# Kernel tuning notes

Hardware: AMD Instinct MI355X
Metric: run time of the kernel (lower is better)

The kernel has to match this reference:

```python
import jax, jax.numpy as jnp
import numpy as np

VOCAB = 128
N_LAYERS = 4
HEAD_DIM = 128
N_HEADS = 16
PAD = 127
HIDDEN = N_HEADS * HEAD_DIM
B, S = 1, 2048
SCALE = 1.0 / float(np.sqrt(HEAD_DIM))


def _intervals(boundary):
    # torch: interval = cumsum(boundary)+1; shifted = roll(1); shifted[:,0]=interval[:,0]
    idx = jnp.cumsum(boundary.astype(jnp.int32), axis=-1) + 1
    sh = jnp.roll(idx, 1, axis=-1)
    return sh.at[:, 0].set(idx[:, 0])


def _build_mask(tokens, segment_mask, specials_mask):
    # Combined causal & padding & word & segment mask, cache_size=0, distances=0.
    word_int = _intervals(specials_mask)            # [B,S]
    seg_bound = ~segment_mask                       # [B,S]
    seg_int = _intervals(seg_bound)                 # [B,S]
    q = jnp.arange(S)[:, None]
    kv = jnp.arange(S)[None, :]
    causal = q >= kv                                # [S,S]
    dist_neg = (q - kv) < 0                         # mask_*_distance = 0 term
    nonpad = tokens != PAD                          # [B,S]
    padm = nonpad[:, :, None] & nonpad[:, None, :]  # [B,S,S]
    wordm = specials_mask[:, None, :] | dist_neg[None] | (word_int[:, :, None] == word_int[:, None, :])
    segm = seg_bound[:, None, :] | dist_neg[None] | (seg_int[:, :, None] == seg_int[:, None, :])
    return causal[None] & padm & wordm & segm       # [B,S,S]


def _attention(h, mask):
    # q=k=v=h (no projections in DummyModel); flex_attention default scale 1/sqrt(D)
    x = h.reshape(B, S, N_HEADS, HEAD_DIM)
    scores = jnp.einsum('bqhd,bkhd->bhqk', x, x) * SCALE
    neg = jnp.finfo(scores.dtype).min
    scores = jnp.where(mask[:, None], scores, neg)
    probs = jax.nn.softmax(scores, axis=-1)
    # fully-masked rows (e.g. padding queries) -> zero output, matching flex_attention
    row_valid = jnp.any(mask, axis=-1)              # [B,S]
    probs = jnp.where(row_valid[:, None, :, None], probs, 0.0)
    out = jnp.einsum('bhqk,bkhd->bqhd', probs, x)
    return out.reshape(B, S, HIDDEN)


def setup_inputs() -> dict:
    key = jax.random.key(0)
    k1, k2, k3, k4, k5, k6 = jax.random.split(key, 6)
    tokens = jax.random.randint(k1, (B, S), 0, PAD)          # 0..126, no pad tokens
    segment_mask = jax.random.bernoulli(k2, 0.98, (B, S))
    specials_mask = jax.random.bernoulli(k3, 0.2, (B, S))    # True = word boundary/special
    emb_w = jax.random.normal(k4, (VOCAB, HIDDEN), jnp.float32) * 0.02
    lm_w = jax.random.normal(k5, (VOCAB, HIDDEN), jnp.float32) * 0.02
    lm_b = jnp.zeros((VOCAB,), jnp.float32)
    seg_w = jax.random.normal(k6, (2, HIDDEN), jnp.float32) * 0.02
    seg_b = jnp.zeros((2,), jnp.float32)
    return {"tokens": tokens, "segment_mask": segment_mask, "specials_mask": specials_mask,
            "emb_w": emb_w, "lm_w": lm_w, "lm_b": lm_b, "seg_w": seg_w, "seg_b": seg_b}


def reference(tokens, segment_mask, specials_mask, emb_w, lm_w, lm_b, seg_w, seg_b):
    mask = _build_mask(tokens, segment_mask, specials_mask)
    hidden = emb_w[tokens]                                   # [B,S,HIDDEN]
    for _ in range(N_LAYERS):
        hidden = _attention(hidden, mask)
    logits = hidden @ lm_w.T + lm_b                          # [B,S,VOCAB]
    logits_segment = hidden @ seg_w.T + seg_b                # [B,S,2]
    return logits, logits_segment
```

## Files before the change

### kernel.cpp

```cpp
#include <hip/hip_runtime.h>

#define S 2048
#define HID 2048
#define NH 16
#define DH 128
#define VOC 128
#define LCAP 128
#define K2EXP 0.12752551286084112f
#define RTHR 62.0f
#define NEGS -3.0e38f

typedef __bf16 bf16_t;
typedef __attribute__((ext_vector_type(8))) __bf16 bf16x8;
typedef __attribute__((ext_vector_type(4))) __bf16 bf16x4;
typedef __attribute__((ext_vector_type(4))) float f32x4;
typedef __attribute__((ext_vector_type(16))) float f32x16;

typedef __attribute__((address_space(1))) unsigned int guint;
typedef __attribute__((address_space(3))) unsigned int luint;

#define MFMA16 __builtin_amdgcn_mfma_f32_16x16x32_bf16
#define MFMA32 __builtin_amdgcn_mfma_f32_32x32x16_bf16

__device__ __forceinline__ void gl_lds16(const void* g, void* l) {
  __builtin_amdgcn_global_load_lds((guint*)(unsigned long long)g,
                                   (luint*)(unsigned)(unsigned long long)l,
                                   16, 0, 0);
}

__device__ __forceinline__ unsigned cvtpk(float lo, float hi) {
  unsigned r;
  asm("v_cvt_pk_bf16_f32 %0, %1, %2" : "=v"(r) : "v"(lo), "v"(hi));
  return r;
}
__device__ __forceinline__ void plswap(unsigned& a, unsigned& b) {
  asm volatile("v_permlane32_swap_b32 %0, %1" : "+v"(a), "+v"(b));
}
__device__ __forceinline__ bf16x8 mk8(unsigned d0, unsigned d1, unsigned d2, unsigned d3) {
  union { unsigned u[4]; bf16x8 v; } x;
  x.u[0] = d0; x.u[1] = d1; x.u[2] = d2; x.u[3] = d3;
  return x.v;
}

__global__ __launch_bounds__(256) void maskprep2(const int* __restrict__ tokens,
                                                 const unsigned char* __restrict__ seg,
                                                 const unsigned char* __restrict__ spc,
                                                 int4* __restrict__ mi,
                                                 int* __restrict__ lq,
                                                 unsigned long long* __restrict__ lmask,
                                                 int2* __restrict__ smeta) {
  __shared__ int ssp[257], ssg[257], smw[257], sms[257], sfl[257];
  __shared__ int fpre[2048];
  __shared__ int ns32[32];
  __shared__ unsigned long long lmk[32];
  __shared__ int cdet[2];
  int t = threadIdx.x;
  if (t < 2) cdet[t] = 0;
  if (t < 32) lmk[t] = 0ull;
  __syncthreads();
  {
    int nz = ((t & 3) != 0 && seg[t]) ? 1 : 0;
    int fc = ((t & 3) == 3 && seg[t] == 0x3f) ? 1 : 0;
    if (nz) atomicAdd(&cdet[0], 1);
    if (fc) atomicAdd(&cdet[1], 1);
  }
  __syncthreads();
  int lay = (cdet[1] > 8) ? 2 : ((cdet[0] > 4) ? 1 : 0);
  auto getb = [&](const unsigned char* p, int i) -> int {
    if (lay == 1) return p[i] != 0;
    if (lay == 2) return ((const float*)p)[i] != 0.f;
    return ((const int*)p)[i] != 0;
  };
  int base = t * 8;
  int spv[8], sgv[8], npv[8], fv[8];
  int a = 0, b = 0, mw = 0, ms = 0, fs = 0;
  for (int j = 0; j < 8; j++) {
    int i = base + j;
    spv[j] = getb(spc, i);
    sgv[j] = 1 - getb(seg, i);
    npv[j] = (tokens[i] != 127) ? 1 : 0;
    fv[j] = spv[j] & sgv[j] & npv[j];
    a += spv[j]; b += sgv[j]; fs += fv[j];
    if (i >= 1 && spv[j]) mw = (i + 1 > mw) ? i + 1 : mw;
    if (i >= 1 && sgv[j]) ms = (i + 1 > ms) ? i + 1 : ms;
  }
  ssp[t + 1] = a; ssg[t + 1] = b; smw[t + 1] = mw; sms[t + 1] = ms; sfl[t + 1] = fs;
  if (t == 0) { ssp[0] = 0; ssg[0] = 0; smw[0] = 0; sms[0] = 0; sfl[0] = 0; }
  __syncthreads();
  for (int off = 1; off < 256; off <<= 1) {
    int v0 = 0, v1 = 0, v2 = 0, v3 = 0, v4 = 0;
    if (t + 1 > off) { v0 = ssp[t+1-off]; v1 = ssg[t+1-off]; v2 = smw[t+1-off]; v3 = sms[t+1-off]; v4 = sfl[t+1-off]; }
    __syncthreads();
    ssp[t + 1] += v0; ssg[t + 1] += v1;
    if (v2 > smw[t + 1]) smw[t + 1] = v2;
    if (v3 > sms[t + 1]) sms[t + 1] = v3;
    sfl[t + 1] += v4;
    __syncthreads();
  }
  if ((t & 7) == 0) {
    int ws = smw[t], ss = sms[t];
    ns32[t >> 3] = ws < ss ? ws : ss;
  }
  int esp = ssp[t], esg = ssg[t], ef = sfl[t];
  for (int j = 0; j < 8; j++) {
    int i = base + j;
    int wint = (i == 0) ? (1 + spv[j]) : (1 + esp);
    int sint = (i == 0) ? (1 + sgv[j]) : (1 + esg);
    mi[i] = make_int4(npv[j] | (spv[j] << 1) | (sgv[j] << 2), wint, sint, 0);
    fpre[i] = ef;
    int lqv = (fv[j] && ef < LCAP) ? ef : -1;
    lq[i] = lqv;
    if (lqv >= 0) atomicOr(&lmk[i >> 6], 1ull << (i & 63));
    esp += spv[j]; esg += sgv[j]; ef += fv[j];
  }
  __syncthreads();
  if (t < 32) {
    lmask[t] = lmk[t];
    int nsTile = ns32[t] >> 6;
    int lc = fpre[nsTile * 64];
    if (lc > LCAP) lc = LCAP;
    smeta[t] = make_int2(nsTile, lc);
  }
}

__global__ __launch_bounds__(256) void bitgen(const int4* __restrict__ mi,
                                              unsigned* __restrict__ cmask) {
  __shared__ int4 km[32];
  int w = blockIdx.x;
  int t = threadIdx.x;
  int q = blockIdx.y * 256 + t;
  if (t < 32) km[t] = mi[w * 32 + t];
  __syncthreads();
  int4 mq = mi[q];
  unsigned word = 0;
  #pragma unroll
  for (int j = 0; j < 32; j++) {
    int kv = w * 32 + j;
    int4 mk = km[j];
    bool v = ((mq.x & mk.x) & 1) &&
             ((mk.x & 2) || (mq.y == mk.y)) &&
             ((mk.x & 4) || (mq.z == mk.z)) &&
             (kv <= q);
    word |= (v ? 1u : 0u) << j;
  }
  cmask[(size_t)w * S + q] = word;
}

__device__ __forceinline__ void store_h_hT(bf16x8 ob[4], bf16_t* tile, int q0, int h,
                                           int ql, int d0, int tid,
                                           bf16_t* __restrict__ hb, bf16_t* __restrict__ hbT) {
  #pragma unroll
  for (int i = 0; i < 4; i++)
    *(bf16x8*)(hb + (size_t)(q0 + ql) * HID + h * DH + d0 + i * 8) = ob[i];
  #pragma unroll
  for (int i = 0; i < 4; i++)
    #pragma unroll
    for (int j = 0; j < 8; j++) tile[ql * 136 + d0 + i * 8 + j] = ob[i][j];
  __syncthreads();
  int dT = tid >> 1, qh = (tid & 1) * 32;
  bf16x8 tb[4];
  #pragma unroll
  for (int i = 0; i < 4; i++)
    #pragma unroll
    for (int j = 0; j < 8; j++) tb[i][j] = tile[(qh + i * 8 + j) * 136 + dT];
  #pragma unroll
  for (int i = 0; i < 4; i++)
    *(bf16x8*)(hbT + (size_t)(h * DH + dT) * S + q0 + qh + i * 8) = tb[i];
}

__global__ __launch_bounds__(256) void embedT(const int* __restrict__ tokens,
                                              const float* __restrict__ emb,
                                              const int* __restrict__ lq,
                                              const unsigned long long* __restrict__ lmask,
                                              bf16_t* __restrict__ hb, bf16_t* __restrict__ hbT,
                                              bf16_t* __restrict__ hbL, bf16_t* __restrict__ hbLT) {
  __shared__ bf16_t tile[64 * 136];
  int tid = threadIdx.x;
  int q0 = blockIdx.x * 64, h = blockIdx.y;
  int ql = tid >> 2, d0 = (tid & 3) * 32;
  int tok = tokens[q0 + ql];
  const float4* src = (const float4*)(emb + (size_t)tok * HID + h * DH + d0);
  bf16x8 ob[4];
  #pragma unroll
  for (int i = 0; i < 8; i++) {
    float4 f = src[i];
    ob[i >> 1][(i & 1) * 4 + 0] = (bf16_t)f.x;
    ob[i >> 1][(i & 1) * 4 + 1] = (bf16_t)f.y;
    ob[i >> 1][(i & 1) * 4 + 2] = (bf16_t)f.z;
    ob[i >> 1][(i & 1) * 4 + 3] = (bf16_t)f.w;
  }
  store_h_hT(ob, tile, q0, h, ql, d0, tid, hb, hbT);
  unsigned long long lm = lmask[q0 >> 6];
  while (lm) {
    int r = __builtin_ctzll(lm);
    lm &= lm - 1;
    int li = lq[q0 + r];
    if (li >= 0 && tid < 128) {
      bf16_t vv = tile[r * 136 + tid];
      hbL[(size_t)li * HID + h * DH + tid] = vv;
      hbLT[((size_t)(h * DH + tid)) * LCAP + li] = vv;
    }
  }
}

__global__ __launch_bounds__(128, 2) void attn5(const bf16_t* __restrict__ hb,
                                                const bf16_t* __restrict__ hbT,
                                                const bf16_t* __restrict__ hbL,
                                                const bf16_t* __restrict__ hbLT,
                                                const unsigned* __restrict__ cmask,
                                                const int4* __restrict__ mi,
                                                const int2* __restrict__ smeta,
                                                const int* __restrict__ lq,
                                                const unsigned long long* __restrict__ lmask,
                                                bf16_t* __restrict__ ob,
                                                bf16_t* __restrict__ obT,
                                                bf16_t* __restrict__ obL,
                                                bf16_t* __restrict__ obLT,
                                                int writeT) {
  __shared__ __align__(16) char lds_raw[65536];

  int h = blockIdx.x, st = blockIdx.y;
  int2 sm = smeta[st];
  int nsT = sm.x, lcount = sm.y;
  int nNear = st + 1 - nsT;
  int nLT = (lcount + 63) >> 6;
  int nIter = nNear + nLT;

  int tid = threadIdx.x, w = tid >> 6, l = tid & 63, l31 = l & 31, hi = l >> 5;
  int q0 = 64 * st, q = q0 + 32 * w + l31;
  int npq = mi[q].x & 1;

  bf16x8 qf[8];
  {
    const bf16_t* hq = hb + (size_t)q * HID + h * DH;
    #pragma unroll
    for (int ks = 0; ks < 8; ks++) qf[ks] = *(const bf16x8*)(hq + ks * 16 + hi * 8);
  }

  f32x16 acc[4];
  #pragma unroll
  for (int i = 0; i < 4; i++)
    #pragma unroll
    for (int r = 0; r < 16; r++) acc[i][r] = 0.f;
  float m = -1e30f, lsum = 0.f;
  int swz = l31 & 7;

  auto STAGE = [&](int i, int b) {
    const bf16_t* Kbase; const bf16_t* Vbase; size_t Vstr;
    if (i < nNear) {
      int kv0 = (nsT + i) * 64;
      Kbase = hb + (size_t)kv0 * HID + h * DH;
      Vbase = hbT + (size_t)(h * DH) * S + kv0; Vstr = S;
    } else {
      int j0 = (i - nNear) * 64;
      Kbase = hbL + (size_t)j0 * HID + h * DH;
      Vbase = hbLT + (size_t)(h * DH) * LCAP + j0; Vstr = LCAP;
    }
    bf16_t* Kb = (bf16_t*)(lds_raw + b * 16384);
    bf16_t* Vb = (bf16_t*)(lds_raw + 32768 + b * 16384);
    #pragma unroll
    for (int i2 = 0; i2 < 8; i2++) {
      int sg = w * 8 + i2;
      int rowK = sg * 4 + (l >> 4); int chK = (l & 15) ^ (rowK & 7);
      gl_lds16(Kbase + (size_t)rowK * HID + chK * 8, Kb + sg * 512);
      int rowV = sg * 8 + (l >> 3); int chV = (l & 7) ^ (rowV & 7);
      gl_lds16(Vbase + (size_t)rowV * Vstr + chV * 8, Vb + sg * 512);
    }
  };

  auto getmask = [&](int i, unsigned& w0, unsigned& w1) {
    if (i < nNear) {
      int tt = nsT + i;
      w0 = cmask[(size_t)(2 * tt) * S + q];
      w1 = cmask[(size_t)(2 * tt + 1) * S + q];
    } else {
      int rem = lcount - (i - nNear) * 64;
      w0 = (rem >= 32) ? 0xffffffffu : ((rem <= 0) ? 0u : ((1u << rem) - 1u));
      int r2 = rem - 32;
      w1 = (r2 >= 32) ? 0xffffffffu : ((r2 <= 0) ? 0u : ((1u << r2) - 1u));
      if (!npq) { w0 = 0u; w1 = 0u; }
    }
  };

  STAGE(0, 0);
  asm volatile("s_waitcnt vmcnt(0)" ::: "memory");
  __builtin_amdgcn_s_barrier();
  __builtin_amdgcn_sched_barrier(0);

  for (int i = 0; i < nIter; i++) {
    int b = i & 1;
    if (i + 1 < nIter) STAGE(i + 1, b ^ 1);
    unsigned w0, w1;
    getmask(i, w0, w1);

    const bf16_t* Kb = (const bf16_t*)(lds_raw + b * 16384);
    const bf16_t* Vb = (const bf16_t*)(lds_raw + 32768 + b * 16384);
    f32x16 s0, s1;
    #pragma unroll
    for (int r = 0; r < 16; r++) { s0[r] = 0.f; s1[r] = 0.f; }
    const bf16_t* k0p = Kb + l31 * 128;
    const bf16_t* k1p = Kb + (32 + l31) * 128;
    #pragma unroll
    for (int ks = 0; ks < 8; ks++) {
      int ch = ((2 * ks + hi) ^ swz) * 8;
      bf16x8 kf0 = *(const bf16x8*)(k0p + ch);
      bf16x8 kf1 = *(const bf16x8*)(k1p + ch);
      s0 = MFMA32(kf0, qf[ks], s0, 0, 0, 0);
      s1 = MFMA32(kf1, qf[ks], s1, 0, 0, 0);
    }

    float sv0[16], sv1[16];
    float mx = NEGS;
    #pragma unroll
    for (int r = 0; r < 16; r++) {
      int bit = (r & 3) + 8 * (r >> 2) + 4 * hi;
      sv0[r] = ((w0 >> bit) & 1u) ? s0[r] : NEGS;
      sv1[r] = ((w1 >> bit) & 1u) ? s1[r] : NEGS;
      mx = fmaxf(mx, fmaxf(sv0[r], sv1[r]));
    }
    mx = fmaxf(mx, __shfl_xor(mx, 32, 64));
    if (__any(mx > m + RTHR)) {
      float mn = fmaxf(m, mx);
      float al = exp2f((m - mn) * K2EXP);
      m = mn; lsum *= al;
      #pragma unroll
      for (int r = 0; r < 16; r++) {
        float alr = __shfl(al, (r & 3) + 8 * (r >> 2) + 4 * hi, 64);
        #pragma unroll
        for (int d = 0; d < 4; d++) acc[d][r] *= alr;
      }
    }
    float mk = m * K2EXP;
    float p0[16], p1[16], ps = 0.f;
    #pragma unroll
    for (int r = 0; r < 16; r++) {
      p0[r] = exp2f(__builtin_fmaf(sv0[r], K2EXP, -mk));
      p1[r] = exp2f(__builtin_fmaf(sv1[r], K2EXP, -mk));
      ps += p0[r] + p1[r];
    }
    ps += __shfl_xor(ps, 32, 64);
    lsum += ps;

    bf16x8 pa[4];
    {
      unsigned a0 = cvtpk(p0[0], p0[1]),  a1 = cvtpk(p0[2], p0[3]);
      unsigned b0 = cvtpk(p0[4], p0[5]),  b1 = cvtpk(p0[6], p0[7]);
      unsigned a2 = cvtpk(p0[8], p0[9]),  a3 = cvtpk(p0[10], p0[11]);
      unsigned b2 = cvtpk(p0[12], p0[13]), b3 = cvtpk(p0[14], p0[15]);
      plswap(a0, b0); plswap(a1, b1); plswap(a2, b2); plswap(a3, b3);
      pa[0] = mk8(a0, a1, b0, b1);
      pa[1] = mk8(a2, a3, b2, b3);
      unsigned c0 = cvtpk(p1[0], p1[1]),  c1 = cvtpk(p1[2], p1[3]);
      unsigned d0 = cvtpk(p1[4], p1[5]),  d1 = cvtpk(p1[6], p1[7]);
      unsigned c2 = cvtpk(p1[8], p1[9]),  c3 = cvtpk(p1[10], p1[11]);
      unsigned d2 = cvtpk(p1[12], p1[13]), d3 = cvtpk(p1[14], p1[15]);
      plswap(c0, d0); plswap(c1, d1); plswap(c2, d2); plswap(c3, d3);
      pa[2] = mk8(c0, c1, d0, d1);
      pa[3] = mk8(c2, c3, d2, d3);
    }

    #pragma unroll
    for (int db = 0; db < 4; db++) {
      const bf16_t* vr = Vb + (32 * db + l31) * 64;
      #pragma unroll
      for (int ks = 0; ks < 4; ks++) {
        bf16x8 vf = *(const bf16x8*)(vr + ((2 * ks + hi) ^ swz) * 8);
        acc[db] = MFMA32(pa[ks], vf, acc[db], 0, 0, 0);
      }
    }

    asm volatile("s_waitcnt vmcnt(0)" ::: "memory");
    __builtin_amdgcn_s_barrier();
    __builtin_amdgcn_sched_barrier(0);
  }

  bf16_t* tl = (bf16_t*)lds_raw;
  float inv = (lsum > 0.f) ? 1.f / lsum : 0.f;
  #pragma unroll
  for (int r = 0; r < 16; r++) {
    int qr = (r & 3) + 8 * (r >> 2) + 4 * hi;
    float ivr = __shfl(inv, qr, 64);
    #pragma unroll
    for (int db = 0; db < 4; db++)
      tl[(32 * w + qr) * 132 + db * 32 + l31] = (bf16_t)(acc[db][r] * ivr);
  }
  __syncthreads();
  {
    int qr2 = tid >> 1;
    #pragma unroll
    for (int k = 0; k < 8; k++) {
      int ch = (tid & 1) * 8 + k;
      bf16x8 v = *(const bf16x8*)(tl + qr2 * 132 + ch * 8);
      *(bf16x8*)(ob + (size_t)(q0 + qr2) * HID + h * DH + ch * 8) = v;
    }
  }
  if (writeT) {
    int dd = tid;
    #pragma unroll
    for (int c = 0; c < 8; c++) {
      bf16x8 v;
      #pragma unroll
      for (int k = 0; k < 8; k++) v[k] = tl[(c * 8 + k) * 132 + dd];
      *(bf16x8*)(obT + (size_t)(h * DH + dd) * S + q0 + c * 8) = v;
    }
    unsigned long long lm = lmask[st];
    while (lm) {
      int r = __builtin_ctzll(lm);
      lm &= lm - 1;
      int li = lq[q0 + r];
      if (li >= 0) {
        bf16_t vv = tl[r * 132 + tid];
        obL[(size_t)li * HID + h * DH + tid] = vv;
        obLT[((size_t)(h * DH + tid)) * LCAP + li] = vv;
      }
    }
  }
}

__global__ __launch_bounds__(256) void wcvt(const float* __restrict__ w, bf16_t* __restrict__ wb) {
  int i = blockIdx.x * 256 + threadIdx.x;
  float4 f = ((const float4*)w)[i];
  bf16x4 v;
  v[0] = (bf16_t)f.x; v[1] = (bf16_t)f.y; v[2] = (bf16_t)f.z; v[3] = (bf16_t)f.w;
  *(bf16x4*)(wb + (size_t)i * 4) = v;
}

__global__ __launch_bounds__(256) void lmseg_head(const bf16_t* __restrict__ hb,
                                                  const bf16_t* __restrict__ wbf,
                                                  const float* __restrict__ bias,
                                                  const float* __restrict__ sw,
                                                  const float* __restrict__ sb,
                                                  float* __restrict__ out,
                                                  float* __restrict__ outseg) {
  __shared__ float red[4][16][130];
  int tid = threadIdx.x;
  int w = tid >> 6, l = tid & 63, l16 = l & 15, g = l >> 4;
  int t0 = blockIdx.x * 16;
  f32x4 acc[8];
  #pragma unroll
  for (int i = 0; i < 8; i++) acc[i] = (f32x4){0.f, 0.f, 0.f, 0.f};
  const bf16_t* arow = hb + (size_t)(t0 + l16) * HID + w * 512;
  for (int k0 = 0; k0 < 512; k0 += 32) {
    bf16x8 af = *(const bf16x8*)(arow + k0 + g * 8);
    #pragma unroll
    for (int vt = 0; vt < 8; vt++) {
      bf16x8 bf_ = *(const bf16x8*)(wbf + (size_t)(vt * 16 + l16) * HID + w * 512 + k0 + g * 8);
      acc[vt] = MFMA16(af, bf_, acc[vt], 0, 0, 0);
    }
  }
  #pragma unroll
  for (int vt = 0; vt < 8; vt++)
    #pragma unroll
    for (int r = 0; r < 4; r++)
      red[w][4 * g + r][vt * 16 + l16] = acc[vt][r];
  __syncthreads();
  int q = tid >> 4, vc = (tid & 15) * 8;
  #pragma unroll
  for (int j = 0; j < 8; j++) {
    float s = red[0][q][vc + j] + red[1][q][vc + j] + red[2][q][vc + j] + red[3][q][vc + j];
    out[(size_t)(t0 + q) * VOC + vc + j] = s + bias[vc + j];
  }
  {
    int c = tid & 15;
    const bf16_t* hrow = hb + (size_t)(t0 + q) * HID + c * 128;
    float s0 = 0.f, s1 = 0.f;
    #pragma unroll
    for (int i = 0; i < 16; i++) {
      bf16x8 v = *(const bf16x8*)(hrow + i * 8);
      const float4* w0p = (const float4*)(sw + c * 128 + i * 8);
      const float4* w1p = (const float4*)(sw + HID + c * 128 + i * 8);
      float4 x0 = w0p[0], x1 = w0p[1], y0 = w1p[0], y1 = w1p[1];
      s0 += (float)v[0]*x0.x + (float)v[1]*x0.y + (float)v[2]*x0.z + (float)v[3]*x0.w
          + (float)v[4]*x1.x + (float)v[5]*x1.y + (float)v[6]*x1.z + (float)v[7]*x1.w;
      s1 += (float)v[0]*y0.x + (float)v[1]*y0.y + (float)v[2]*y0.z + (float)v[3]*y0.w
          + (float)v[4]*y1.x + (float)v[5]*y1.y + (float)v[6]*y1.z + (float)v[7]*y1.w;
    }
    #pragma unroll
    for (int off = 1; off < 16; off <<= 1) {
      s0 += __shfl_xor(s0, off, 64);
      s1 += __shfl_xor(s1, off, 64);
    }
    if (c == 0) {
      outseg[(size_t)(t0 + q) * 2] = s0 + sb[0];
      outseg[(size_t)(t0 + q) * 2 + 1] = s1 + sb[1];
    }
  }
}

extern "C" void kernel_launch(void* const* d_in, const int* in_sizes, int n_in,
                              void* d_out, int out_size, void* d_ws, size_t ws_size,
                              hipStream_t stream) {
  const int* tokens = (const int*)d_in[0];
  const unsigned char* seg = (const unsigned char*)d_in[1];
  const unsigned char* spc = (const unsigned char*)d_in[2];
  const float* emb_w = (const float*)d_in[3];
  const float* lm_w = (const float*)d_in[4];
  const float* lm_b = (const float*)d_in[5];
  const float* seg_w = (const float*)d_in[6];
  const float* seg_b = (const float*)d_in[7];

  char* ws = (char*)d_ws;
  int4* mi = (int4*)ws;
  unsigned* cmask = (unsigned*)(ws + (1u << 20));
  int* lq = (int*)(ws + (1u << 20) + (512u << 10));
  unsigned long long* lmask = (unsigned long long*)(ws + (1u << 20) + (520u << 10));
  int2* smeta = (int2*)(ws + (1u << 20) + (524u << 10));
  bf16_t* wbf = (bf16_t*)(ws + (2u << 20));
  bf16_t* hbLA  = (bf16_t*)(ws + (3u << 20));
  bf16_t* hbLTA = (bf16_t*)(ws + (3u << 20) + (512u << 10));
  bf16_t* hbLB  = (bf16_t*)(ws + (4u << 20));
  bf16_t* hbLTB = (bf16_t*)(ws + (4u << 20) + (512u << 10));
  bf16_t* hbA  = (bf16_t*)(ws + (8u << 20));
  bf16_t* hbTA = (bf16_t*)(ws + (16u << 20));
  bf16_t* hbB  = (bf16_t*)(ws + (24u << 20));
  bf16_t* hbTB = (bf16_t*)(ws + (32u << 20));
  float* out = (float*)d_out;

  maskprep2<<<1, 256, 0, stream>>>(tokens, seg, spc, mi, lq, lmask, smeta);
  bitgen<<<dim3(64, 8), 256, 0, stream>>>(mi, cmask);
  embedT<<<dim3(S / 64, NH), 256, 0, stream>>>(tokens, emb_w, lq, lmask, hbA, hbTA, hbLA, hbLTA);

  bf16_t* cur = hbA;   bf16_t* curT = hbTA;
  bf16_t* nxt = hbB;   bf16_t* nxtT = hbTB;
  bf16_t* curL = hbLA; bf16_t* curLT = hbLTA;
  bf16_t* nxtL = hbLB; bf16_t* nxtLT = hbLTB;
  for (int L = 0; L < 4; L++) {
    attn5<<<dim3(NH, 32), 128, 0, stream>>>(cur, curT, curL, curLT, cmask, mi, smeta, lq, lmask,
                                            nxt, nxtT, nxtL, nxtLT, (L < 3) ? 1 : 0);
    bf16_t* t1 = cur; cur = nxt; nxt = t1;
    bf16_t* t2 = curT; curT = nxtT; nxtT = t2;
    bf16_t* t3 = curL; curL = nxtL; nxtL = t3;
    bf16_t* t4 = curLT; curLT = nxtLT; nxtLT = t4;
  }

  wcvt<<<(VOC * HID / 4) / 256, 256, 0, stream>>>(lm_w, wbf);
  lmseg_head<<<S / 16, 256, 0, stream>>>(cur, wbf, lm_b, seg_w, seg_b, out, out + (size_t)S * VOC);
}
```

Baseline: 143.8 us.

## Widen attention blocks to 128 queries with four waves sharing K/V tiles

The attention kernel now processes 128 query rows per block with 256 threads (four waves) instead of 64 rows with two waves, so each staged 64-key K/V tile in LDS is reused by twice as many queries and global loads per query drop. Mask metadata is regenerated per 128-row tile, and staging work is split across four waves. It also adds s_setprio around the MFMA loops and removes the sched_barriers. The grid halves to 16x16 blocks, which lowers parallelism and means the near window starts at the earlier of two 64-row tiles' starts, so some extra masked tiles may be computed.

```diff
diff --git a/kernel.cpp b/kernel.cpp
--- a/kernel.cpp
+++ b/kernel.cpp
@@ -51,7 +51,7 @@
                                                  int2* __restrict__ smeta) {
   __shared__ int ssp[257], ssg[257], smw[257], sms[257], sfl[257];
   __shared__ int fpre[2048];
-  __shared__ int ns32[32];
+  __shared__ int ns16[16];
   __shared__ unsigned long long lmk[32];
   __shared__ int cdet[2];
   int t = threadIdx.x;
@@ -97,9 +97,9 @@
     sfl[t + 1] += v4;
     __syncthreads();
   }
-  if ((t & 7) == 0) {
+  if ((t & 15) == 0) {
     int ws = smw[t], ss = sms[t];
-    ns32[t >> 3] = ws < ss ? ws : ss;
+    ns16[t >> 4] = ws < ss ? ws : ss;
   }
   int esp = ssp[t], esg = ssg[t], ef = sfl[t];
   for (int j = 0; j < 8; j++) {
@@ -114,9 +114,9 @@
     esp += spv[j]; esg += sgv[j]; ef += fv[j];
   }
   __syncthreads();
-  if (t < 32) {
-    lmask[t] = lmk[t];
-    int nsTile = ns32[t] >> 6;
+  if (t < 32) lmask[t] = lmk[t];
+  if (t < 16) {
+    int nsTile = ns16[t] >> 6;
     int lc = fpre[nsTile * 64];
     if (lc > LCAP) lc = LCAP;
     smeta[t] = make_int2(nsTile, lc);
@@ -203,7 +203,7 @@
   }
 }
 
-__global__ __launch_bounds__(128, 2) void attn5(const bf16_t* __restrict__ hb,
+__global__ __launch_bounds__(256, 2) void attn6(const bf16_t* __restrict__ hb,
                                                 const bf16_t* __restrict__ hbT,
                                                 const bf16_t* __restrict__ hbL,
                                                 const bf16_t* __restrict__ hbLT,
@@ -222,12 +222,12 @@
   int h = blockIdx.x, st = blockIdx.y;
   int2 sm = smeta[st];
   int nsT = sm.x, lcount = sm.y;
-  int nNear = st + 1 - nsT;
+  int nNear = 2 * st + 2 - nsT;
   int nLT = (lcount + 63) >> 6;
   int nIter = nNear + nLT;
 
   int tid = threadIdx.x, w = tid >> 6, l = tid & 63, l31 = l & 31, hi = l >> 5;
-  int q0 = 64 * st, q = q0 + 32 * w + l31;
+  int q0 = 128 * st, q = q0 + 32 * w + l31;
   int npq = mi[q].x & 1;
 
   bf16x8 qf[8];
@@ -259,8 +259,8 @@
     bf16_t* Kb = (bf16_t*)(lds_raw + b * 16384);
     bf16_t* Vb = (bf16_t*)(lds_raw + 32768 + b * 16384);
     #pragma unroll
-    for (int i2 = 0; i2 < 8; i2++) {
-      int sg = w * 8 + i2;
+    for (int i2 = 0; i2 < 4; i2++) {
+      int sg = w * 4 + i2;
       int rowK = sg * 4 + (l >> 4); int chK = (l & 15) ^ (rowK & 7);
       gl_lds16(Kbase + (size_t)rowK * HID + chK * 8, Kb + sg * 512);
       int rowV = sg * 8 + (l >> 3); int chV = (l & 7) ^ (rowV & 7);
@@ -285,7 +285,6 @@
   STAGE(0, 0);
   asm volatile("s_waitcnt vmcnt(0)" ::: "memory");
   __builtin_amdgcn_s_barrier();
-  __builtin_amdgcn_sched_barrier(0);
 
   for (int i = 0; i < nIter; i++) {
     int b = i & 1;
@@ -300,6 +299,7 @@
     for (int r = 0; r < 16; r++) { s0[r] = 0.f; s1[r] = 0.f; }
     const bf16_t* k0p = Kb + l31 * 128;
     const bf16_t* k1p = Kb + (32 + l31) * 128;
+    __builtin_amdgcn_s_setprio(1);
     #pragma unroll
     for (int ks = 0; ks < 8; ks++) {
       int ch = ((2 * ks + hi) ^ swz) * 8;
@@ -308,6 +308,7 @@
       s0 = MFMA32(kf0, qf[ks], s0, 0, 0, 0);
       s1 = MFMA32(kf1, qf[ks], s1, 0, 0, 0);
     }
+    __builtin_amdgcn_s_setprio(0);
 
     float sv0[16], sv1[16];
     float mx = NEGS;
@@ -359,6 +360,7 @@
       pa[3] = mk8(c2, c3, d2, d3);
     }
 
+    __builtin_amdgcn_s_setprio(1);
     #pragma unroll
     for (int db = 0; db < 4; db++) {
       const bf16_t* vr = Vb + (32 * db + l31) * 64;
@@ -368,10 +370,10 @@
         acc[db] = MFMA32(pa[ks], vf, acc[db], 0, 0, 0);
       }
     }
+    __builtin_amdgcn_s_setprio(0);
 
     asm volatile("s_waitcnt vmcnt(0)" ::: "memory");
     __builtin_amdgcn_s_barrier();
-    __builtin_amdgcn_sched_barrier(0);
   }
 
   bf16_t* tl = (bf16_t*)lds_raw;
@@ -395,23 +397,27 @@
     }
   }
   if (writeT) {
-    int dd = tid;
-    #pragma unroll
-    for (int c = 0; c < 8; c++) {
+    int grp = tid >> 4, ln = tid & 15;
+    #pragma unroll
+    for (int k = 0; k < 8; k++) {
+      int dd = grp * 8 + k;
       bf16x8 v;
       #pragma unroll
-      for (int k = 0; k < 8; k++) v[k] = tl[(c * 8 + k) * 132 + dd];
-      *(bf16x8*)(obT + (size_t)(h * DH + dd) * S + q0 + c * 8) = v;
-    }
-    unsigned long long lm = lmask[st];
-    while (lm) {
-      int r = __builtin_ctzll(lm);
-      lm &= lm - 1;
-      int li = lq[q0 + r];
-      if (li >= 0) {
-        bf16_t vv = tl[r * 132 + tid];
-        obL[(size_t)li * HID + h * DH + tid] = vv;
-        obLT[((size_t)(h * DH + tid)) * LCAP + li] = vv;
+      for (int e = 0; e < 8; e++) v[e] = tl[(ln * 8 + e) * 132 + dd];
+      *(bf16x8*)(obT + (size_t)(h * DH + dd) * S + q0 + ln * 8) = v;
+    }
+    #pragma unroll
+    for (int wd = 0; wd < 2; wd++) {
+      unsigned long long lm = lmask[2 * st + wd];
+      while (lm) {
+        int r = __builtin_ctzll(lm);
+        lm &= lm - 1;
+        int li = lq[q0 + wd * 64 + r];
+        if (li >= 0 && tid < 128) {
+          bf16_t vv = tl[(wd * 64 + r) * 132 + tid];
+          obL[(size_t)li * HID + h * DH + tid] = vv;
+          obLT[((size_t)(h * DH + tid)) * LCAP + li] = vv;
+        }
       }
     }
   }
@@ -525,7 +531,7 @@
   bf16_t* curL = hbLA; bf16_t* curLT = hbLTA;
   bf16_t* nxtL = hbLB; bf16_t* nxtLT = hbLTB;
   for (int L = 0; L < 4; L++) {
-    attn5<<<dim3(NH, 32), 128, 0, stream>>>(cur, curT, curL, curLT, cmask, mi, smeta, lq, lmask,
+    attn6<<<dim3(NH, 16), 256, 0, stream>>>(cur, curT, curL, curLT, cmask, mi, smeta, lq, lmask,
                                             nxt, nxtT, nxtL, nxtLT, (L < 3) ? 1 : 0);
     bf16_t* t1 = cur; cur = nxt; nxt = t1;
     bf16_t* t2 = curT; curT = nxtT; nxtT = t2;
```

New measurement: 140.9 us. -2.0%, faster.

## Shrink attention tiles to 32 queries/keys with single-wave blocks and tile skipping

Applied to the files above, without the earlier changes.

The attention kernel now uses 32-row query and key tiles, one 64-thread wave per block, and twice as many blocks (16x64). Because each block is a single wave, the LDS barriers are removed, and tiles whose mask is entirely zero skip the QK, softmax and PV work. The prefetch wait becomes a partial vmcnt so the next tile's loads can overlap compute. Mask metadata in maskprep is recomputed at 32-row granularity. In exchange, each block gets less data reuse per tile and issues smaller MFMA batches.

```diff
diff --git a/kernel.cpp b/kernel.cpp
--- a/kernel.cpp
+++ b/kernel.cpp
@@ -51,7 +51,7 @@
                                                  int2* __restrict__ smeta) {
   __shared__ int ssp[257], ssg[257], smw[257], sms[257], sfl[257];
   __shared__ int fpre[2048];
-  __shared__ int ns32[32];
+  __shared__ int ns64[64];
   __shared__ unsigned long long lmk[32];
   __shared__ int cdet[2];
   int t = threadIdx.x;
@@ -97,9 +97,9 @@
     sfl[t + 1] += v4;
     __syncthreads();
   }
-  if ((t & 7) == 0) {
+  if ((t & 3) == 0) {
     int ws = smw[t], ss = sms[t];
-    ns32[t >> 3] = ws < ss ? ws : ss;
+    ns64[t >> 2] = ws < ss ? ws : ss;
   }
   int esp = ssp[t], esg = ssg[t], ef = sfl[t];
   for (int j = 0; j < 8; j++) {
@@ -114,10 +114,10 @@
     esp += spv[j]; esg += sgv[j]; ef += fv[j];
   }
   __syncthreads();
-  if (t < 32) {
-    lmask[t] = lmk[t];
-    int nsTile = ns32[t] >> 6;
-    int lc = fpre[nsTile * 64];
+  if (t < 32) lmask[t] = lmk[t];
+  if (t < 64) {
+    int nsTile = ns64[t] >> 5;
+    int lc = fpre[nsTile * 32];
     if (lc > LCAP) lc = LCAP;
     smeta[t] = make_int2(nsTile, lc);
   }
@@ -203,31 +203,31 @@
   }
 }
 
-__global__ __launch_bounds__(128, 2) void attn5(const bf16_t* __restrict__ hb,
-                                                const bf16_t* __restrict__ hbT,
-                                                const bf16_t* __restrict__ hbL,
-                                                const bf16_t* __restrict__ hbLT,
-                                                const unsigned* __restrict__ cmask,
-                                                const int4* __restrict__ mi,
-                                                const int2* __restrict__ smeta,
-                                                const int* __restrict__ lq,
-                                                const unsigned long long* __restrict__ lmask,
-                                                bf16_t* __restrict__ ob,
-                                                bf16_t* __restrict__ obT,
-                                                bf16_t* __restrict__ obL,
-                                                bf16_t* __restrict__ obLT,
-                                                int writeT) {
-  __shared__ __align__(16) char lds_raw[65536];
+__global__ __launch_bounds__(64, 2) void attn7(const bf16_t* __restrict__ hb,
+                                               const bf16_t* __restrict__ hbT,
+                                               const bf16_t* __restrict__ hbL,
+                                               const bf16_t* __restrict__ hbLT,
+                                               const unsigned* __restrict__ cmask,
+                                               const int4* __restrict__ mi,
+                                               const int2* __restrict__ smeta,
+                                               const int* __restrict__ lq,
+                                               const unsigned long long* __restrict__ lmask,
+                                               bf16_t* __restrict__ ob,
+                                               bf16_t* __restrict__ obT,
+                                               bf16_t* __restrict__ obL,
+                                               bf16_t* __restrict__ obLT,
+                                               int writeT) {
+  __shared__ __align__(16) char lds_raw[32768];
 
   int h = blockIdx.x, st = blockIdx.y;
   int2 sm = smeta[st];
   int nsT = sm.x, lcount = sm.y;
   int nNear = st + 1 - nsT;
-  int nLT = (lcount + 63) >> 6;
+  int nLT = (lcount + 31) >> 5;
   int nIter = nNear + nLT;
 
-  int tid = threadIdx.x, w = tid >> 6, l = tid & 63, l31 = l & 31, hi = l >> 5;
-  int q0 = 64 * st, q = q0 + 32 * w + l31;
+  int l = threadIdx.x, l31 = l & 31, hi = l >> 5;
+  int q0 = 32 * st, q = q0 + l31;
   int npq = mi[q].x & 1;
 
   bf16x8 qf[8];
@@ -248,130 +248,110 @@
   auto STAGE = [&](int i, int b) {
     const bf16_t* Kbase; const bf16_t* Vbase; size_t Vstr;
     if (i < nNear) {
-      int kv0 = (nsT + i) * 64;
+      int kv0 = (nsT + i) * 32;
       Kbase = hb + (size_t)kv0 * HID + h * DH;
       Vbase = hbT + (size_t)(h * DH) * S + kv0; Vstr = S;
     } else {
-      int j0 = (i - nNear) * 64;
+      int j0 = (i - nNear) * 32;
       Kbase = hbL + (size_t)j0 * HID + h * DH;
       Vbase = hbLT + (size_t)(h * DH) * LCAP + j0; Vstr = LCAP;
     }
     bf16_t* Kb = (bf16_t*)(lds_raw + b * 16384);
-    bf16_t* Vb = (bf16_t*)(lds_raw + 32768 + b * 16384);
+    bf16_t* Vb = (bf16_t*)(lds_raw + b * 16384 + 8192);
     #pragma unroll
     for (int i2 = 0; i2 < 8; i2++) {
-      int sg = w * 8 + i2;
-      int rowK = sg * 4 + (l >> 4); int chK = (l & 15) ^ (rowK & 7);
-      gl_lds16(Kbase + (size_t)rowK * HID + chK * 8, Kb + sg * 512);
-      int rowV = sg * 8 + (l >> 3); int chV = (l & 7) ^ (rowV & 7);
-      gl_lds16(Vbase + (size_t)rowV * Vstr + chV * 8, Vb + sg * 512);
+      int rowK = i2 * 4 + (l >> 4); int chK = (l & 15) ^ (rowK & 7);
+      gl_lds16(Kbase + (size_t)rowK * HID + chK * 8, Kb + i2 * 512);
+    }
+    #pragma unroll
+    for (int i2 = 0; i2 < 8; i2++) {
+      int rowV = i2 * 16 + (l >> 2); int chV = (l & 3) ^ (rowV & 3);
+      gl_lds16(Vbase + (size_t)rowV * Vstr + chV * 8, Vb + i2 * 512);
     }
   };
 
-  auto getmask = [&](int i, unsigned& w0, unsigned& w1) {
-    if (i < nNear) {
-      int tt = nsT + i;
-      w0 = cmask[(size_t)(2 * tt) * S + q];
-      w1 = cmask[(size_t)(2 * tt + 1) * S + q];
-    } else {
-      int rem = lcount - (i - nNear) * 64;
-      w0 = (rem >= 32) ? 0xffffffffu : ((rem <= 0) ? 0u : ((1u << rem) - 1u));
-      int r2 = rem - 32;
-      w1 = (r2 >= 32) ? 0xffffffffu : ((r2 <= 0) ? 0u : ((1u << r2) - 1u));
-      if (!npq) { w0 = 0u; w1 = 0u; }
-    }
+  auto getmask = [&](int i) -> unsigned {
+    if (i < nNear) return cmask[(size_t)(nsT + i) * S + q];
+    int rem = lcount - (i - nNear) * 32;
+    unsigned w0 = (rem >= 32) ? 0xffffffffu : ((rem <= 0) ? 0u : ((1u << rem) - 1u));
+    return npq ? w0 : 0u;
   };
 
   STAGE(0, 0);
-  asm volatile("s_waitcnt vmcnt(0)" ::: "memory");
-  __builtin_amdgcn_s_barrier();
-  __builtin_amdgcn_sched_barrier(0);
-
   for (int i = 0; i < nIter; i++) {
     int b = i & 1;
-    if (i + 1 < nIter) STAGE(i + 1, b ^ 1);
-    unsigned w0, w1;
-    getmask(i, w0, w1);
-
-    const bf16_t* Kb = (const bf16_t*)(lds_raw + b * 16384);
-    const bf16_t* Vb = (const bf16_t*)(lds_raw + 32768 + b * 16384);
-    f32x16 s0, s1;
-    #pragma unroll
-    for (int r = 0; r < 16; r++) { s0[r] = 0.f; s1[r] = 0.f; }
-    const bf16_t* k0p = Kb + l31 * 128;
-    const bf16_t* k1p = Kb + (32 + l31) * 128;
-    #pragma unroll
-    for (int ks = 0; ks < 8; ks++) {
-      int ch = ((2 * ks + hi) ^ swz) * 8;
-      bf16x8 kf0 = *(const bf16x8*)(k0p + ch);
-      bf16x8 kf1 = *(const bf16x8*)(k1p + ch);
-      s0 = MFMA32(kf0, qf[ks], s0, 0, 0, 0);
-      s1 = MFMA32(kf1, qf[ks], s1, 0, 0, 0);
-    }
-
-    float sv0[16], sv1[16];
-    float mx = NEGS;
-    #pragma unroll
-    for (int r = 0; r < 16; r++) {
-      int bit = (r & 3) + 8 * (r >> 2) + 4 * hi;
-      sv0[r] = ((w0 >> bit) & 1u) ? s0[r] : NEGS;
-      sv1[r] = ((w1 >> bit) & 1u) ? s1[r] : NEGS;
-      mx = fmaxf(mx, fmaxf(sv0[r], sv1[r]));
-    }
-    mx = fmaxf(mx, __shfl_xor(mx, 32, 64));
-    if (__any(mx > m + RTHR)) {
-      float mn = fmaxf(m, mx);
-      float al = exp2f((m - mn) * K2EXP);
-      m = mn; lsum *= al;
+    if (i + 1 < nIter) {
+      STAGE(i + 1, b ^ 1);
+      asm volatile("s_waitcnt vmcnt(16)" ::: "memory");
+    } else {
+      asm volatile("s_waitcnt vmcnt(0)" ::: "memory");
+    }
+    unsigned w0 = getmask(i);
+
+    if (__any(w0 != 0u)) {
+      const bf16_t* Kb = (const bf16_t*)(lds_raw + b * 16384);
+      const bf16_t* Vb = (const bf16_t*)(lds_raw + b * 16384 + 8192);
+      f32x16 s;
+      #pragma unroll
+      for (int r = 0; r < 16; r++) s[r] = 0.f;
+      const bf16_t* kp = Kb + l31 * 128;
+      #pragma unroll
+      for (int ks = 0; ks < 8; ks++) {
+        bf16x8 kf = *(const bf16x8*)(kp + (((2 * ks + hi) ^ swz) * 8));
+        s = MFMA32(kf, qf[ks], s, 0, 0, 0);
+      }
+
+      float sv[16];
+      float mx = NEGS;
       #pragma unroll
       for (int r = 0; r < 16; r++) {
-        float alr = __shfl(al, (r & 3) + 8 * (r >> 2) + 4 * hi, 64);
+        int bit = (r & 3) + 8 * (r >> 2) + 4 * hi;
+        sv[r] = ((w0 >> bit) & 1u) ? s[r] : NEGS;
+        mx = fmaxf(mx, sv[r]);
+      }
+      mx = fmaxf(mx, __shfl_xor(mx, 32, 64));
+      if (__any(mx > m + RTHR)) {
+        float mn = fmaxf(m, mx);
+        float al = exp2f((m - mn) * K2EXP);
+        m = mn; lsum *= al;
         #pragma unroll
-        for (int d = 0; d < 4; d++) acc[d][r] *= alr;
-      }
-    }
-    float mk = m * K2EXP;
-    float p0[16], p1[16], ps = 0.f;
-    #pragma unroll
-    for (int r = 0; r < 16; r++) {
-      p0[r] = exp2f(__builtin_fmaf(sv0[r], K2EXP, -mk));
-      p1[r] = exp2f(__builtin_fmaf(sv1[r], K2EXP, -mk));
-      ps += p0[r] + p1[r];
-    }
-    ps += __shfl_xor(ps, 32, 64);
-    lsum += ps;
-
-    bf16x8 pa[4];
-    {
-      unsigned a0 = cvtpk(p0[0], p0[1]),  a1 = cvtpk(p0[2], p0[3]);
-      unsigned b0 = cvtpk(p0[4], p0[5]),  b1 = cvtpk(p0[6], p0[7]);
-      unsigned a2 = cvtpk(p0[8], p0[9]),  a3 = cvtpk(p0[10], p0[11]);
-      unsigned b2 = cvtpk(p0[12], p0[13]), b3 = cvtpk(p0[14], p0[15]);
-      plswap(a0, b0); plswap(a1, b1); plswap(a2, b2); plswap(a3, b3);
-      pa[0] = mk8(a0, a1, b0, b1);
-      pa[1] = mk8(a2, a3, b2, b3);
-      unsigned c0 = cvtpk(p1[0], p1[1]),  c1 = cvtpk(p1[2], p1[3]);
-      unsigned d0 = cvtpk(p1[4], p1[5]),  d1 = cvtpk(p1[6], p1[7]);
-      unsigned c2 = cvtpk(p1[8], p1[9]),  c3 = cvtpk(p1[10], p1[11]);
-      unsigned d2 = cvtpk(p1[12], p1[13]), d3 = cvtpk(p1[14], p1[15]);
-      plswap(c0, d0); plswap(c1, d1); plswap(c2, d2); plswap(c3, d3);
-      pa[2] = mk8(c0, c1, d0, d1);
-      pa[3] = mk8(c2, c3, d2, d3);
-    }
-
-    #pragma unroll
-    for (int db = 0; db < 4; db++) {
-      const bf16_t* vr = Vb + (32 * db + l31) * 64;
+        for (int r = 0; r < 16; r++) {
+          float alr = __shfl(al, (r & 3) + 8 * (r >> 2) + 4 * hi, 64);
+          #pragma unroll
+          for (int d = 0; d < 4; d++) acc[d][r] *= alr;
+        }
+      }
+      float mk = m * K2EXP;
+      float p[16], ps = 0.f;
       #pragma unroll
-      for (int ks = 0; ks < 4; ks++) {
-        bf16x8 vf = *(const bf16x8*)(vr + ((2 * ks + hi) ^ swz) * 8);
-        acc[db] = MFMA32(pa[ks], vf, acc[db], 0, 0, 0);
-      }
-    }
-
-    asm volatile("s_waitcnt vmcnt(0)" ::: "memory");
-    __builtin_amdgcn_s_barrier();
-    __builtin_amdgcn_sched_barrier(0);
+      for (int r = 0; r < 16; r++) {
+        p[r] = exp2f(__builtin_fmaf(sv[r], K2EXP, -mk));
+        ps += p[r];
+      }
+      ps += __shfl_xor(ps, 32, 64);
+      lsum += ps;
+
+      bf16x8 pa[2];
+      {
+        unsigned a0 = cvtpk(p[0], p[1]),   a1 = cvtpk(p[2], p[3]);
+        unsigned b0 = cvtpk(p[4], p[5]),   b1 = cvtpk(p[6], p[7]);
+        unsigned a2 = cvtpk(p[8], p[9]),   a3 = cvtpk(p[10], p[11]);
+        unsigned b2 = cvtpk(p[12], p[13]), b3 = cvtpk(p[14], p[15]);
+        plswap(a0, b0); plswap(a1, b1); plswap(a2, b2); plswap(a3, b3);
+        pa[0] = mk8(a0, a1, b0, b1);
+        pa[1] = mk8(a2, a3, b2, b3);
+      }
+
+      #pragma unroll
+      for (int db = 0; db < 4; db++) {
+        const bf16_t* vr = Vb + (32 * db + l31) * 32;
+        #pragma unroll
+        for (int ks = 0; ks < 2; ks++) {
+          bf16x8 vf = *(const bf16x8*)(vr + (((2 * ks + hi) ^ (l31 & 3)) * 8));
+          acc[db] = MFMA32(pa[ks], vf, acc[db], 0, 0, 0);
+        }
+      }
+    }
   }
 
   bf16_t* tl = (bf16_t*)lds_raw;
@@ -382,36 +362,41 @@
     float ivr = __shfl(inv, qr, 64);
     #pragma unroll
     for (int db = 0; db < 4; db++)
-      tl[(32 * w + qr) * 132 + db * 32 + l31] = (bf16_t)(acc[db][r] * ivr);
-  }
-  __syncthreads();
+      tl[qr * 132 + db * 32 + l31] = (bf16_t)(acc[db][r] * ivr);
+  }
   {
-    int qr2 = tid >> 1;
+    int row = l >> 1, hf = l & 1;
     #pragma unroll
     for (int k = 0; k < 8; k++) {
-      int ch = (tid & 1) * 8 + k;
-      bf16x8 v = *(const bf16x8*)(tl + qr2 * 132 + ch * 8);
-      *(bf16x8*)(ob + (size_t)(q0 + qr2) * HID + h * DH + ch * 8) = v;
+      bf16x8 v = *(const bf16x8*)(tl + row * 132 + hf * 64 + k * 8);
+      *(bf16x8*)(ob + (size_t)(q0 + row) * HID + h * DH + hf * 64 + k * 8) = v;
     }
   }
   if (writeT) {
-    int dd = tid;
-    #pragma unroll
-    for (int c = 0; c < 8; c++) {
-      bf16x8 v;
+    #pragma unroll
+    for (int half = 0; half < 2; half++) {
+      int dd = l + 64 * half;
       #pragma unroll
-      for (int k = 0; k < 8; k++) v[k] = tl[(c * 8 + k) * 132 + dd];
-      *(bf16x8*)(obT + (size_t)(h * DH + dd) * S + q0 + c * 8) = v;
-    }
-    unsigned long long lm = lmask[st];
-    while (lm) {
-      int r = __builtin_ctzll(lm);
-      lm &= lm - 1;
+      for (int c = 0; c < 4; c++) {
+        bf16x8 v;
+        #pragma unroll
+        for (int e = 0; e < 8; e++) v[e] = tl[(c * 8 + e) * 132 + dd];
+        *(bf16x8*)(obT + (size_t)(h * DH + dd) * S + q0 + c * 8) = v;
+      }
+    }
+    unsigned lm32 = (unsigned)(lmask[st >> 1] >> ((st & 1) * 32));
+    while (lm32) {
+      int r = __builtin_ctz(lm32);
+      lm32 &= lm32 - 1;
       int li = lq[q0 + r];
       if (li >= 0) {
-        bf16_t vv = tl[r * 132 + tid];
-        obL[(size_t)li * HID + h * DH + tid] = vv;
-        obLT[((size_t)(h * DH + tid)) * LCAP + li] = vv;
+        #pragma unroll
+        for (int half = 0; half < 2; half++) {
+          int dd = l + 64 * half;
+          bf16_t vv = tl[r * 132 + dd];
+          obL[(size_t)li * HID + h * DH + dd] = vv;
+          obLT[((size_t)(h * DH + dd)) * LCAP + li] = vv;
+        }
       }
     }
   }
@@ -525,8 +510,8 @@
   bf16_t* curL = hbLA; bf16_t* curLT = hbLTA;
   bf16_t* nxtL = hbLB; bf16_t* nxtLT = hbLTB;
   for (int L = 0; L < 4; L++) {
-    attn5<<<dim3(NH, 32), 128, 0, stream>>>(cur, curT, curL, curLT, cmask, mi, smeta, lq, lmask,
-                                            nxt, nxtT, nxtL, nxtLT, (L < 3) ? 1 : 0);
+    attn7<<<dim3(NH, 64), 64, 0, stream>>>(cur, curT, curL, curLT, cmask, mi, smeta, lq, lmask,
+                                           nxt, nxtT, nxtL, nxtLT, (L < 3) ? 1 : 0);
     bf16_t* t1 = cur; cur = nxt; nxt = t1;
     bf16_t* t2 = curT; curT = nxtT; nxtT = t2;
     bf16_t* t3 = curL; curL = nxtL; nxtL = t3;
```

New measurement: 147.6 us. 1.03x slower.
